# Optimization experiments

Measured on AMD Instinct MI355X. Metric: run time of the kernel, lower is better.

Reference implementation:

```python
import jax, jax.numpy as jnp
import numpy as np
import math

B, S, DM, H = 2, 2048, 1024, 16
DH = DM // H  # 64


def setup_inputs() -> dict:
    key = jax.random.key(0)
    ks = jax.random.split(key, 12)
    s = 1.0 / math.sqrt(DM)
    inp = {
        "key": jax.random.normal(ks[0], (B, S, DM), jnp.float32),
        "value": jax.random.normal(ks[1], (B, S, DM), jnp.float32),
        "query": jax.random.normal(ks[2], (B, S, DM), jnp.float32),
        # causal mask: True = masked out (matches masked_fill semantics)
        "mask": jnp.broadcast_to(~jnp.tril(jnp.ones((S, S), bool)), (B, S, S)),
        "Wk": jax.random.normal(ks[3], (DM, DM), jnp.float32) * s,
        "bk": jnp.zeros((DM,), jnp.float32),
        "Wv": jax.random.normal(ks[4], (DM, DM), jnp.float32) * s,
        "bv": jnp.zeros((DM,), jnp.float32),
        "Wq": jax.random.normal(ks[5], (DM, DM), jnp.float32) * s,
        "bq": jnp.zeros((DM,), jnp.float32),
        "Wo": jax.random.normal(ks[6], (DM, DM), jnp.float32) * s,
        "bo": jnp.zeros((DM,), jnp.float32),
    }
    return inp


def _split_heads(x):
    # [B, S, H*DH] -> [B, H, S, DH]
    b, s, _ = x.shape
    return x.reshape(b, s, H, DH).transpose(0, 2, 1, 3)


def reference(key, value, query, mask, Wk, bk, Wv, bv, Wq, bq, Wo, bo):
    key_up = _split_heads(key @ Wk.T + bk)      # [B,H,S,DH]
    value_up = _split_heads(value @ Wv.T + bv)  # [B,H,S,DH]
    query_up = _split_heads(query @ Wq.T + bq) / math.sqrt(DH)
    scores = jnp.einsum("bhqd,bhkd->bhqk", query_up, key_up)  # [B,H,S,S]
    scores = jnp.where(mask[:, None, :, :], jnp.float32(-1e18), scores)
    attn = jax.nn.softmax(scores, axis=-1)
    # dropout is identity in eval mode
    context = jnp.einsum("bhqk,bhkd->bhqd", attn, value_up)
    context = context.transpose(0, 2, 1, 3).reshape(key.shape[0], -1, H * DH)
    output = context @ Wo.T + bo                # [B,S,DM]
    top_attn = attn[:, 0, :, :]                 # [B,S,S]
    return output, top_attn
```

## Files before the change

### kernel.cpp

```cpp
#include <hip/hip_runtime.h>
#include <hip/hip_bf16.h>
#include <math.h>

#define B_ 2
#define S_ 2048
#define DM_ 1024
#define H_ 16
#define DH_ 64

using short8 = __attribute__((ext_vector_type(8))) short;
using f32x4  = __attribute__((ext_vector_type(4))) float;

typedef const __attribute__((address_space(1))) void* gas_cvp;
typedef __attribute__((address_space(3))) void* las_vp;

struct CvtJobs {
    const float* in[7];
    ushort* out[7];
};

__device__ __forceinline__ ushort f2bu(float x) {
    __hip_bfloat16 h = __float2bfloat16(x);
    return *(ushort*)&h;
}

__global__ __launch_bounds__(256) void cvt_bf16(CvtJobs jobs) {
    const int bid = blockIdx.x;
    int j, blk;
    if (bid < 6144) { j = bid >> 11; blk = bid & 2047; }
    else { const int r = bid - 6144; j = 3 + (r >> 9); blk = r & 511; }
    const int idx = (blk * 256 + threadIdx.x) * 8;
    const float* in = jobs.in[j];
    float4 a = *(const float4*)&in[idx];
    float4 b = *(const float4*)&in[idx + 4];
    ushort u[8];
    u[0] = f2bu(a.x); u[1] = f2bu(a.y); u[2] = f2bu(a.z); u[3] = f2bu(a.w);
    u[4] = f2bu(b.x); u[5] = f2bu(b.y); u[6] = f2bu(b.z); u[7] = f2bu(b.w);
    *(int4*)&jobs.out[j][idx] = *(int4*)u;
}

struct ProjJobs {
    const ushort* A[3];
    const ushort* W[3];
    const float* bias[3];
    ushort* C[3];
    float scale[3];
};

#define PSTAGE_A(buf, k0v)                                                     \
    {                                                                          \
        _Pragma("unroll")                                                      \
        for (int i = 0; i < 2; i++) {                                          \
            const int s   = i * 512 + tid;                                     \
            const int c   = s >> 8;                                            \
            const int row = s & 255;                                           \
            __builtin_amdgcn_global_load_lds(                                  \
                (gas_cvp)(Ag + (size_t)(i0 + row) * 1024 + (k0v) + c * 8),     \
                (las_vp)&SH[(buf) * 16384 + (i * 512 + w * 64) * 8], 16, 0, 0);\
        }                                                                      \
    }

#define PSTAGE_B(buf, k0v)                                                     \
    {                                                                          \
        _Pragma("unroll")                                                      \
        for (int i = 0; i < 2; i++) {                                          \
            const int s   = i * 512 + tid;                                     \
            const int c   = s >> 8;                                            \
            const int row = s & 255;                                           \
            __builtin_amdgcn_global_load_lds(                                  \
                (gas_cvp)(Wg + (size_t)(j0 + row) * 1024 + (k0v) + c * 8),     \
                (las_vp)&SH[(buf) * 16384 + 8192 + (i * 512 + w * 64) * 8],    \
                16, 0, 0);                                                     \
        }                                                                      \
    }

__global__ __launch_bounds__(512) void gemm_proj3(ProjJobs jobs)
{
    __shared__ ushort SH[65536];

    const int o   = blockIdx.x;
    const int swz = (o & 7) * 24 + (o >> 3);
    const int z   = swz >> 6;
    const int rem = swz & 63;
    const int by  = rem >> 2;
    const int bx  = rem & 3;

    const ushort* Ag = jobs.A[z];
    const ushort* Wg = jobs.W[z];
    const float* bias = jobs.bias[z];
    ushort* C = jobs.C[z];
    const float scale = jobs.scale[z];

    const int tid  = threadIdx.x;
    const int w    = tid >> 6;
    const int lane = tid & 63;
    const int g    = lane >> 4;
    const int lr   = lane & 15;
    const int wm   = w >> 2;
    const int wn   = w & 3;
    const int i0   = by * 256;
    const int j0   = bx * 256;

    f32x4 acc[8][4];
    #pragma unroll
    for (int m = 0; m < 8; m++)
        #pragma unroll
        for (int n = 0; n < 4; n++)
            #pragma unroll
            for (int jj = 0; jj < 4; jj++) acc[m][n][jj] = 0.f;

    PSTAGE_A(0, 0);  PSTAGE_B(0, 0);
    PSTAGE_A(1, 32); PSTAGE_B(1, 32);
    PSTAGE_A(2, 64); PSTAGE_B(2, 64);

    for (int kt = 0; kt < 32; kt++) {
        if (kt < 30)       asm volatile("s_waitcnt vmcnt(8)" ::: "memory");
        else if (kt == 30) asm volatile("s_waitcnt vmcnt(4)" ::: "memory");
        else               asm volatile("s_waitcnt vmcnt(0)" ::: "memory");
        __builtin_amdgcn_s_barrier();

        const int ab = (kt & 3) * 16384;

        short8 af[8], bf01[2];
        #pragma unroll
        for (int m = 0; m < 8; m++)
            af[m] = *(const short8*)&SH[ab + (g * 256 + wm * 128 + m * 16 + lr) * 8];
        #pragma unroll
        for (int n = 0; n < 2; n++)
            bf01[n] = *(const short8*)&SH[ab + 8192 + (g * 256 + wn * 64 + n * 16 + lr) * 8];
        if (kt + 3 < 32) PSTAGE_A((kt + 3) & 3, (kt + 3) * 32);

        __builtin_amdgcn_s_setprio(1);
        #pragma unroll
        for (int m = 0; m < 8; m++)
            #pragma unroll
            for (int n = 0; n < 2; n++)
                acc[m][n] = __builtin_amdgcn_mfma_f32_16x16x32_bf16(
                    af[m], bf01[n], acc[m][n], 0, 0, 0);
        __builtin_amdgcn_s_setprio(0);
        __builtin_amdgcn_s_barrier();

        short8 bf23[2];
        #pragma unroll
        for (int n = 0; n < 2; n++)
            bf23[n] = *(const short8*)&SH[ab + 8192 + (g * 256 + wn * 64 + (n + 2) * 16 + lr) * 8];
        if (kt + 3 < 32) PSTAGE_B((kt + 3) & 3, (kt + 3) * 32);

        __builtin_amdgcn_s_setprio(1);
        #pragma unroll
        for (int m = 0; m < 8; m++)
            #pragma unroll
            for (int n = 0; n < 2; n++)
                acc[m][n + 2] = __builtin_amdgcn_mfma_f32_16x16x32_bf16(
                    af[m], bf23[n], acc[m][n + 2], 0, 0, 0);
        __builtin_amdgcn_s_setprio(0);
    }

    const int colbase = j0 + wn * 64;
    const int rowbase = i0 + wm * 128;
    #pragma unroll
    for (int n = 0; n < 4; n++) {
        const int col = colbase + n * 16 + lr;
        const float bb = bias[col];
        const int hh = col >> 6;
        const int d = col & 63;
        #pragma unroll
        for (int m = 0; m < 8; m++) {
            const int rb = rowbase + m * 16 + g * 4;
            #pragma unroll
            for (int jj = 0; jj < 4; jj++) {
                const float v = (acc[m][n][jj] + bb) * scale;
                const int i = rb + jj;
                const int b = i >> 11;
                const int srow = i & 2047;
                C[(((size_t)b * H_ + hh) * S_ + srow) * DH_ + d] = f2bu(v);
            }
        }
    }
}

#define GEMM_STAGE_A(buf, k0v)                                                 \
    {                                                                          \
        _Pragma("unroll")                                                      \
        for (int i = 0; i < 2; i++) {                                          \
            const int s   = i * 256 + tid;                                     \
            const int c   = s >> 7;                                            \
            const int row = s & 127;                                           \
            __builtin_amdgcn_global_load_lds(                                  \
                (gas_cvp)(Ag + (size_t)(i0 + row) * 1024 + (k0v) + c * 8),     \
                (las_vp)&AsB[buf][0][(i * 256 + w * 64) * 8], 16, 0, 0);       \
        }                                                                      \
    }

#define GEMM_STAGE_B(buf, k0v)                                                 \
    {                                                                          \
        _Pragma("unroll")                                                      \
        for (int i = 0; i < 2; i++) {                                          \
            const int s   = i * 256 + tid;                                     \
            const int c   = s >> 7;                                            \
            const int row = s & 127;                                           \
            __builtin_amdgcn_global_load_lds(                                  \
                (gas_cvp)(Wg + (size_t)(j0 + row) * 1024 + (k0v) + c * 8),     \
                (las_vp)&AsB[buf][1][(i * 256 + w * 64) * 8], 16, 0, 0);       \
        }                                                                      \
    }

__global__ __launch_bounds__(512) void flash_mfma(
    const ushort* __restrict__ Qb, const ushort* __restrict__ Kb,
    const ushort* __restrict__ Vb, __hip_bfloat16* __restrict__ ctx,
    float* __restrict__ m0, float* __restrict__ l0)
{
    const int bid = blockIdx.x;
    const int xcd = bid & 7;
    const int t   = bid >> 3;
    const int P   = (t >> 3) * 8 + xcd;
    const int p   = t & 7;
    const int h   = P & 15;
    const int b   = P >> 4;

    const size_t hoff = ((size_t)b * H_ + h) * S_ * DH_;
    const ushort* Qh = Qb + hoff;
    const ushort* Kh = Kb + hoff;
    const ushort* Vh = Vb + hoff;

    __shared__ ushort Ks[64][72];
    __shared__ ushort Vt[64][72];
    __shared__ ushort Ps[8][16][72];

    const int tid  = threadIdx.x;
    const int w    = tid >> 6;
    const int lane = tid & 63;
    const int g    = lane >> 4;
    const int lr   = lane & 15;
    const int q0A  = p * 128 + w * 16;
    const int q0B  = (15 - p) * 128 + w * 16;
    const int diagA = (q0A + 15) >> 6;
    const int diagB = (q0B + 15) >> 6;
    const int nkt   = 2 * (16 - p);

    short8 qfA0, qfA1, qfB0, qfB1;
    {
        const ushort* qa = Qh + (size_t)(q0A + lr) * DH_ + g * 8;
        qfA0 = *(const short8*)(qa);
        qfA1 = *(const short8*)(qa + 32);
        const ushort* qb = Qh + (size_t)(q0B + lr) * DH_ + g * 8;
        qfB0 = *(const short8*)(qb);
        qfB1 = *(const short8*)(qb + 32);
    }

    f32x4 oA[4], oB[4];
    #pragma unroll
    for (int nc = 0; nc < 4; nc++) {
        oA[nc][0]=0.f; oA[nc][1]=0.f; oA[nc][2]=0.f; oA[nc][3]=0.f;
        oB[nc][0]=0.f; oB[nc][1]=0.f; oB[nc][2]=0.f; oB[nc][3]=0.f;
    }
    float mA = -1e30f, lA = 0.f;
    float mB = -1e30f, lB = 0.f;

    int4 pk = *(const int4*)(Kh + (size_t)lane * DH_ + w * 8);
    int4 pv = *(const int4*)(Vh + (size_t)lane * DH_ + w * 8);

    for (int kt = 0; kt < nkt; kt++) {
        const int kvb = kt * 64;
        __syncthreads();
        {
            *(int4*)&Ks[lane][w * 8] = pk;
            ushort vv[8];
            *(int4*)vv = pv;
            #pragma unroll
            for (int j2 = 0; j2 < 8; j2++) Vt[w * 8 + j2][lane] = vv[j2];
        }
        if (kt + 1 < nkt) {
            const size_t roff = (size_t)(kvb + 64 + lane) * DH_ + w * 8;
            pk = *(const int4*)(Kh + roff);
            pv = *(const int4*)(Vh + roff);
        }
        __syncthreads();

        #pragma unroll
        for (int u = 0; u < 2; u++) {
            const int diag = (u == 0) ? diagA : diagB;
            if (kt > diag) continue;
            const int q0w   = (u == 0) ? q0A : q0B;
            const short8 qf0 = (u == 0) ? qfA0 : qfB0;
            const short8 qf1 = (u == 0) ? qfA1 : qfB1;
            float& m_r = (u == 0) ? mA : mB;
            float& l_r = (u == 0) ? lA : lB;
            f32x4* o   = (u == 0) ? oA : oB;
            const int qglob = q0w + lr;

            f32x4 st[4];
            #pragma unroll
            for (int mt = 0; mt < 4; mt++) { st[mt][0]=0.f; st[mt][1]=0.f; st[mt][2]=0.f; st[mt][3]=0.f; }
            __builtin_amdgcn_s_setprio(1);
            #pragma unroll
            for (int mt = 0; mt < 4; mt++) {
                short8 ka = *(const short8*)&Ks[16 * mt + lr][8 * g];
                short8 kb = *(const short8*)&Ks[16 * mt + lr][32 + 8 * g];
                st[mt] = __builtin_amdgcn_mfma_f32_16x16x32_bf16(ka, qf0, st[mt], 0, 0, 0);
                st[mt] = __builtin_amdgcn_mfma_f32_16x16x32_bf16(kb, qf1, st[mt], 0, 0, 0);
            }
            __builtin_amdgcn_s_setprio(0);

            if (kt == diag) {
                #pragma unroll
                for (int mt = 0; mt < 4; mt++)
                    #pragma unroll
                    for (int jj = 0; jj < 4; jj++)
                        if (kvb + 16 * mt + 4 * g + jj > qglob) st[mt][jj] = -1e30f;
            }

            float pmax = st[0][0];
            #pragma unroll
            for (int mt = 0; mt < 4; mt++)
                #pragma unroll
                for (int jj = 0; jj < 4; jj++)
                    pmax = fmaxf(pmax, st[mt][jj]);
            pmax = fmaxf(pmax, __shfl_xor(pmax, 16));
            pmax = fmaxf(pmax, __shfl_xor(pmax, 32));

            const bool defer = __all(pmax - m_r <= 8.0f);
            float mnew = m_r, scv = 1.0f;
            if (!defer) {
                mnew = fmaxf(m_r, pmax);
                scv  = __expf(m_r - mnew);
            }

            float lsum = 0.f;
            #pragma unroll
            for (int mt = 0; mt < 4; mt++)
                #pragma unroll
                for (int jj = 0; jj < 4; jj++) {
                    st[mt][jj] = __expf(st[mt][jj] - mnew);
                    lsum += st[mt][jj];
                }
            lsum += __shfl_xor(lsum, 16);
            lsum += __shfl_xor(lsum, 32);
            l_r = l_r * scv + lsum;
            m_r = mnew;

            if (!defer) {
                float sc0 = __shfl(scv, 4 * g + 0);
                float sc1 = __shfl(scv, 4 * g + 1);
                float sc2 = __shfl(scv, 4 * g + 2);
                float sc3 = __shfl(scv, 4 * g + 3);
                #pragma unroll
                for (int nc = 0; nc < 4; nc++) {
                    o[nc][0] *= sc0; o[nc][1] *= sc1;
                    o[nc][2] *= sc2; o[nc][3] *= sc3;
                }
            }

            #pragma unroll
            for (int mt = 0; mt < 4; mt++) {
                ushort u4[4];
                #pragma unroll
                for (int jj = 0; jj < 4; jj++) u4[jj] = f2bu(st[mt][jj]);
                *(uint2*)&Ps[w][lr][16 * mt + 4 * g] = *(uint2*)u4;
            }

            short8 pa0 = *(const short8*)&Ps[w][lr][8 * g];
            short8 pa1 = *(const short8*)&Ps[w][lr][32 + 8 * g];
            __builtin_amdgcn_s_setprio(1);
            #pragma unroll
            for (int nc = 0; nc < 4; nc++) {
                short8 v0 = *(const short8*)&Vt[16 * nc + lr][8 * g];
                short8 v1 = *(const short8*)&Vt[16 * nc + lr][32 + 8 * g];
                o[nc] = __builtin_amdgcn_mfma_f32_16x16x32_bf16(pa0, v0, o[nc], 0, 0, 0);
                o[nc] = __builtin_amdgcn_mfma_f32_16x16x32_bf16(pa1, v1, o[nc], 0, 0, 0);
            }
            __builtin_amdgcn_s_setprio(0);
        }
    }

    #pragma unroll
    for (int u = 0; u < 2; u++) {
        const int q0w = (u == 0) ? q0A : q0B;
        const float m_r = (u == 0) ? mA : mB;
        const float l_r = (u == 0) ? lA : lB;
        const f32x4* o  = (u == 0) ? oA : oB;
        const float linv = 1.0f / l_r;
        float li0 = __shfl(linv, 4 * g + 0);
        float li1 = __shfl(linv, 4 * g + 1);
        float li2 = __shfl(linv, 4 * g + 2);
        float li3 = __shfl(linv, 4 * g + 3);
        #pragma unroll
        for (int reg = 0; reg < 4; reg++) {
            const int qrow = q0w + 4 * g + reg;
            const float li = (reg == 0) ? li0 : (reg == 1) ? li1 : (reg == 2) ? li2 : li3;
            __hip_bfloat16* cp = ctx + ((size_t)b * S_ + qrow) * DM_ + h * DH_;
            #pragma unroll
            for (int nc = 0; nc < 4; nc++)
                cp[16 * nc + lr] = __float2bfloat16(o[nc][reg] * li);
        }
        if (h == 0 && lane < 16) {
            m0[b * S_ + q0w + lane] = m_r;
            l0[b * S_ + q0w + lane] = l_r;
        }
    }
}

__global__ __launch_bounds__(256) void tail_fused(
    const ushort* __restrict__ ctxb, const ushort* __restrict__ Wg_,
    const float* __restrict__ bo, float* __restrict__ out,
    const ushort* __restrict__ Qb, const ushort* __restrict__ Kb,
    const float* __restrict__ m0, const float* __restrict__ l0,
    float* __restrict__ attn)
{
    __shared__ ushort AsB[3][2][4096];
    const int o = blockIdx.x;
    const int tid = threadIdx.x;
    const int w    = tid >> 6;
    const int lane = tid & 63;
    const int g    = lane >> 4;
    const int lr   = lane & 15;

    if (o < 256) {
        const int swz = (o & 7) * 32 + (o >> 3);
        const int by  = swz >> 3;
        const int bx  = swz & 7;
        const int wm  = w >> 1;
        const int wn  = w & 1;
        const int i0  = by * 128;
        const int j0  = bx * 128;
        const ushort* Ag = ctxb;
        const ushort* Wg = Wg_;

        f32x4 acc[4][4];
        #pragma unroll
        for (int m = 0; m < 4; m++)
            #pragma unroll
            for (int n = 0; n < 4; n++)
                #pragma unroll
                for (int jj = 0; jj < 4; jj++) acc[m][n][jj] = 0.f;

        int bufc = 0;
        GEMM_STAGE_A(0, 0);  GEMM_STAGE_B(0, 0);
        GEMM_STAGE_A(1, 32); GEMM_STAGE_B(1, 32);
        for (int k0 = 0; k0 < 1024; k0 += 32) {
            if (k0 + 32 < 1024)
                asm volatile("s_waitcnt vmcnt(4)" ::: "memory");
            else
                asm volatile("s_waitcnt vmcnt(0)" ::: "memory");
            __builtin_amdgcn_s_barrier();
            const int nb = (bufc + 2 >= 3) ? bufc - 1 : bufc + 2;

            short8 af[4], bf01[2];
            #pragma unroll
            for (int m = 0; m < 4; m++)
                af[m] = *(const short8*)&AsB[bufc][0][((g << 7) + wm * 64 + m * 16 + lr) * 8];
            #pragma unroll
            for (int n = 0; n < 2; n++)
                bf01[n] = *(const short8*)&AsB[bufc][1][((g << 7) + wn * 64 + n * 16 + lr) * 8];
            if (k0 + 64 < 1024) GEMM_STAGE_A(nb, k0 + 64);

            __builtin_amdgcn_s_setprio(1);
            #pragma unroll
            for (int m = 0; m < 4; m++)
                #pragma unroll
                for (int n = 0; n < 2; n++)
                    acc[m][n] = __builtin_amdgcn_mfma_f32_16x16x32_bf16(
                        af[m], bf01[n], acc[m][n], 0, 0, 0);
            __builtin_amdgcn_s_setprio(0);
            __builtin_amdgcn_s_barrier();

            short8 bf23[2];
            #pragma unroll
            for (int n = 0; n < 2; n++)
                bf23[n] = *(const short8*)&AsB[bufc][1][((g << 7) + wn * 64 + (n + 2) * 16 + lr) * 8];
            if (k0 + 64 < 1024) GEMM_STAGE_B(nb, k0 + 64);

            __builtin_amdgcn_s_setprio(1);
            #pragma unroll
            for (int m = 0; m < 4; m++)
                #pragma unroll
                for (int n = 0; n < 2; n++)
                    acc[m][n + 2] = __builtin_amdgcn_mfma_f32_16x16x32_bf16(
                        af[m], bf23[n], acc[m][n + 2], 0, 0, 0);
            __builtin_amdgcn_s_setprio(0);

            bufc = (bufc + 1 == 3) ? 0 : bufc + 1;
        }

        const int colbase = j0 + wn * 64;
        const int rowbase = i0 + wm * 64;
        #pragma unroll
        for (int n = 0; n < 4; n++) {
            const int col = colbase + n * 16 + lr;
            const float bb = bo[col];
            #pragma unroll
            for (int m = 0; m < 4; m++) {
                const int rb = rowbase + m * 16 + g * 4;
                #pragma unroll
                for (int jj = 0; jj < 4; jj++)
                    out[(size_t)(rb + jj) * DM_ + col] = acc[m][n][jj] + bb;
            }
        }
        return;
    }

    const int t   = o - 256;
    const int kt  = t & 31;
    const int qt2 = (t >> 5) & 31;
    const int b   = t >> 10;
    float* ap = attn + (size_t)b * S_ * S_;

    if (kt > qt2) {
        const int row = qt2 * 64 + (tid >> 2);
        const int col = kt * 64 + (tid & 3) * 16;
        float4 z = {0.f, 0.f, 0.f, 0.f};
        float* rp = ap + (size_t)row * S_ + col;
        *(float4*)&rp[0]  = z;
        *(float4*)&rp[4]  = z;
        *(float4*)&rp[8]  = z;
        *(float4*)&rp[12] = z;
        return;
    }

    ushort (*Ks)[72] = (ushort(*)[72])&AsB[0][0][0];
    const int q0w = qt2 * 64 + w * 16;
    const int kvb = kt * 64;
    const size_t hoff = (size_t)b * H_ * S_ * DH_;
    const ushort* Qh = Qb + hoff;
    const ushort* Kh = Kb + hoff;

    #pragma unroll
    for (int i = 0; i < 2; i++) {
        const int c = w + 4 * i;
        int4 k4 = *(const int4*)(Kh + (size_t)(kvb + lane) * DH_ + c * 8);
        *(int4*)&Ks[lane][c * 8] = k4;
    }

    short8 qf0, qf1;
    {
        const ushort* qp = Qh + (size_t)(q0w + lr) * DH_ + g * 8;
        qf0 = *(const short8*)(qp);
        qf1 = *(const short8*)(qp + 32);
    }
    const int qglob = q0w + lr;
    const float mv   = m0[b * S_ + qglob];
    const float linv = 1.0f / l0[b * S_ + qglob];
    __syncthreads();

    f32x4 st[4];
    #pragma unroll
    for (int mt = 0; mt < 4; mt++) { st[mt][0]=0.f; st[mt][1]=0.f; st[mt][2]=0.f; st[mt][3]=0.f; }
    #pragma unroll
    for (int mt = 0; mt < 4; mt++) {
        short8 ka = *(const short8*)&Ks[16 * mt + lr][8 * g];
        short8 kb = *(const short8*)&Ks[16 * mt + lr][32 + 8 * g];
        st[mt] = __builtin_amdgcn_mfma_f32_16x16x32_bf16(ka, qf0, st[mt], 0, 0, 0);
        st[mt] = __builtin_amdgcn_mfma_f32_16x16x32_bf16(kb, qf1, st[mt], 0, 0, 0);
    }

    float* rowp = ap + (size_t)qglob * S_ + kvb;
    #pragma unroll
    for (int mt = 0; mt < 4; mt++) {
        float4 ov;
        float v[4];
        #pragma unroll
        for (int jj = 0; jj < 4; jj++) {
            const int kv = 16 * mt + 4 * g + jj;
            float pv = __expf(st[mt][jj] - mv) * linv;
            v[jj] = (kvb + kv > qglob) ? 0.f : pv;
        }
        ov.x = v[0]; ov.y = v[1]; ov.z = v[2]; ov.w = v[3];
        *(float4*)&rowp[16 * mt + 4 * g] = ov;
    }
}

extern "C" void kernel_launch(void* const* d_in, const int* in_sizes, int n_in,
                              void* d_out, int out_size, void* d_ws, size_t ws_size,
                              hipStream_t stream)
{
    const float* key   = (const float*)d_in[0];
    const float* value = (const float*)d_in[1];
    const float* query = (const float*)d_in[2];
    const float* Wk = (const float*)d_in[4];
    const float* bk = (const float*)d_in[5];
    const float* Wv = (const float*)d_in[6];
    const float* bv = (const float*)d_in[7];
    const float* Wq = (const float*)d_in[8];
    const float* bq = (const float*)d_in[9];
    const float* Wo = (const float*)d_in[10];
    const float* bo = (const float*)d_in[11];

    char* ws = (char*)d_ws;
    const size_t per = (size_t)B_ * H_ * S_ * DH_;
    const size_t wsz = (size_t)DM_ * DM_;
    __hip_bfloat16* Qp   = (__hip_bfloat16*)ws;
    __hip_bfloat16* Kp   = Qp + per;
    __hip_bfloat16* Vp   = Kp + per;
    __hip_bfloat16* ctxb = Vp + per;
    __hip_bfloat16* qc   = ctxb + per;
    __hip_bfloat16* kc   = qc + per;
    __hip_bfloat16* vc   = kc + per;
    __hip_bfloat16* wqb  = vc + per;
    __hip_bfloat16* wkb  = wqb + wsz;
    __hip_bfloat16* wvb  = wkb + wsz;
    __hip_bfloat16* wob  = wvb + wsz;
    float* m0 = (float*)(wob + wsz);
    float* l0 = m0 + B_ * S_;

    float* out   = (float*)d_out;
    float* topat = out + (size_t)B_ * S_ * DM_;

    CvtJobs jobs;
    jobs.in[0] = query; jobs.out[0] = (ushort*)qc;
    jobs.in[1] = key;   jobs.out[1] = (ushort*)kc;
    jobs.in[2] = value; jobs.out[2] = (ushort*)vc;
    jobs.in[3] = Wq;    jobs.out[3] = (ushort*)wqb;
    jobs.in[4] = Wk;    jobs.out[4] = (ushort*)wkb;
    jobs.in[5] = Wv;    jobs.out[5] = (ushort*)wvb;
    jobs.in[6] = Wo;    jobs.out[6] = (ushort*)wob;
    cvt_bf16<<<6144 + 4 * 512, 256, 0, stream>>>(jobs);

    ProjJobs pj;
    pj.A[0] = (const ushort*)qc; pj.W[0] = (const ushort*)wqb; pj.bias[0] = bq;
    pj.C[0] = (ushort*)Qp; pj.scale[0] = 0.125f;
    pj.A[1] = (const ushort*)kc; pj.W[1] = (const ushort*)wkb; pj.bias[1] = bk;
    pj.C[1] = (ushort*)Kp; pj.scale[1] = 1.0f;
    pj.A[2] = (const ushort*)vc; pj.W[2] = (const ushort*)wvb; pj.bias[2] = bv;
    pj.C[2] = (ushort*)Vp; pj.scale[2] = 1.0f;
    gemm_proj3<<<192, 512, 0, stream>>>(pj);

    flash_mfma<<<256, 512, 0, stream>>>(
        (const ushort*)Qp, (const ushort*)Kp, (const ushort*)Vp, ctxb, m0, l0);

    tail_fused<<<256 + B_ * 32 * 32, 256, 0, stream>>>(
        (const ushort*)ctxb, (const ushort*)wob, bo, out,
        (const ushort*)Qp, (const ushort*)Kp, m0, l0, topat);
}
```

Baseline: 137.7 us.

## Split flash attention KV range in two halves and merge with combine kernel

The flash attention kernel now splits each block's key range into two halves processed by separate blocks, doubling the grid from 256 to 512. Each half writes unnormalized bf16 partial outputs plus row max and sum into reused workspace buffers. A new combine kernel merges the two partials with log-sum-exp rescaling and writes ctx and the head-0 stats. This aims to fill more compute units, at the cost of an extra launch, extra global traffic and bf16 rounding of the unnormalized partials.

```diff
diff --git a/kernel.cpp b/kernel.cpp
--- a/kernel.cpp
+++ b/kernel.cpp
@@ -207,16 +207,23 @@
 
 __global__ __launch_bounds__(512) void flash_mfma(
     const ushort* __restrict__ Qb, const ushort* __restrict__ Kb,
-    const ushort* __restrict__ Vb, __hip_bfloat16* __restrict__ ctx,
-    float* __restrict__ m0, float* __restrict__ l0)
+    const ushort* __restrict__ Vb,
+    ushort* __restrict__ po0, ushort* __restrict__ po1,
+    float* __restrict__ pm0, float* __restrict__ pm1,
+    float* __restrict__ pl0, float* __restrict__ pl1)
 {
     const int bid = blockIdx.x;
     const int xcd = bid & 7;
     const int t   = bid >> 3;
-    const int P   = (t >> 3) * 8 + xcd;
+    const int P   = (t >> 4) * 8 + xcd;
+    const int s   = (t >> 3) & 1;
     const int p   = t & 7;
     const int h   = P & 15;
     const int b   = P >> 4;
+
+    ushort* po = s ? po1 : po0;
+    float*  pm = s ? pm1 : pm0;
+    float*  pl = s ? pl1 : pl0;
 
     const size_t hoff = ((size_t)b * H_ + h) * S_ * DH_;
     const ushort* Qh = Qb + hoff;
@@ -236,7 +243,9 @@
     const int q0B  = (15 - p) * 128 + w * 16;
     const int diagA = (q0A + 15) >> 6;
     const int diagB = (q0B + 15) >> 6;
-    const int nkt   = 2 * (16 - p);
+    const int h0    = 16 - p;
+    const int ks    = s * h0;
+    const int ke    = ks + h0;
 
     short8 qfA0, qfA1, qfB0, qfB1;
     {
@@ -257,10 +266,10 @@
     float mA = -1e30f, lA = 0.f;
     float mB = -1e30f, lB = 0.f;
 
-    int4 pk = *(const int4*)(Kh + (size_t)lane * DH_ + w * 8);
-    int4 pv = *(const int4*)(Vh + (size_t)lane * DH_ + w * 8);
-
-    for (int kt = 0; kt < nkt; kt++) {
+    int4 pk = *(const int4*)(Kh + (size_t)(ks * 64 + lane) * DH_ + w * 8);
+    int4 pv = *(const int4*)(Vh + (size_t)(ks * 64 + lane) * DH_ + w * 8);
+
+    for (int kt = ks; kt < ke; kt++) {
         const int kvb = kt * 64;
         __syncthreads();
         {
@@ -270,7 +279,7 @@
             #pragma unroll
             for (int j2 = 0; j2 < 8; j2++) Vt[w * 8 + j2][lane] = vv[j2];
         }
-        if (kt + 1 < nkt) {
+        if (kt + 1 < ke) {
             const size_t roff = (size_t)(kvb + 64 + lane) * DH_ + w * 8;
             pk = *(const int4*)(Kh + roff);
             pv = *(const int4*)(Vh + roff);
@@ -379,24 +388,57 @@
         const float m_r = (u == 0) ? mA : mB;
         const float l_r = (u == 0) ? lA : lB;
         const f32x4* o  = (u == 0) ? oA : oB;
-        const float linv = 1.0f / l_r;
-        float li0 = __shfl(linv, 4 * g + 0);
-        float li1 = __shfl(linv, 4 * g + 1);
-        float li2 = __shfl(linv, 4 * g + 2);
-        float li3 = __shfl(linv, 4 * g + 3);
         #pragma unroll
         for (int reg = 0; reg < 4; reg++) {
             const int qrow = q0w + 4 * g + reg;
-            const float li = (reg == 0) ? li0 : (reg == 1) ? li1 : (reg == 2) ? li2 : li3;
-            __hip_bfloat16* cp = ctx + ((size_t)b * S_ + qrow) * DM_ + h * DH_;
+            ushort* cp = po + ((size_t)P * S_ + qrow) * 64;
             #pragma unroll
             for (int nc = 0; nc < 4; nc++)
-                cp[16 * nc + lr] = __float2bfloat16(o[nc][reg] * li);
-        }
-        if (h == 0 && lane < 16) {
-            m0[b * S_ + q0w + lane] = m_r;
-            l0[b * S_ + q0w + lane] = l_r;
-        }
+                cp[16 * nc + lr] = f2bu(o[nc][reg]);
+        }
+        if (lane < 16) {
+            pm[(size_t)P * S_ + q0w + lane] = m_r;
+            pl[(size_t)P * S_ + q0w + lane] = l_r;
+        }
+    }
+}
+
+__global__ __launch_bounds__(256) void flash_combine(
+    const ushort* __restrict__ po0, const ushort* __restrict__ po1,
+    const float* __restrict__ pm0, const float* __restrict__ pm1,
+    const float* __restrict__ pl0, const float* __restrict__ pl1,
+    ushort* __restrict__ ctx, float* __restrict__ m0, float* __restrict__ l0)
+{
+    const int t   = threadIdx.x;
+    const int row = blockIdx.x * 8 + (t >> 5);
+    const int d0  = (t & 31) * 2;
+    const int P = row >> 11;
+    const int q = row & 2047;
+    const int h = P & 15;
+    const int b = P >> 4;
+
+    const float m1 = pm0[row], m2 = pm1[row];
+    const float l1 = pl0[row], l2 = pl1[row];
+    const float m  = fmaxf(m1, m2);
+    const float f1 = __expf(m1 - m);
+    const float f2 = __expf(m2 - m);
+    const float l  = l1 * f1 + l2 * f2;
+    const float inv = 1.0f / l;
+
+    const uint a = *(const uint*)&po0[(size_t)row * 64 + d0];
+    const uint c = *(const uint*)&po1[(size_t)row * 64 + d0];
+    const float a0 = __uint_as_float((a & 0xffffu) << 16);
+    const float a1 = __uint_as_float((a >> 16) << 16);
+    const float c0 = __uint_as_float((c & 0xffffu) << 16);
+    const float c1 = __uint_as_float((c >> 16) << 16);
+    ushort r[2];
+    r[0] = f2bu((a0 * f1 + c0 * f2) * inv);
+    r[1] = f2bu((a1 * f1 + c1 * f2) * inv);
+    *(uint*)&ctx[((size_t)b * S_ + q) * DM_ + h * 64 + d0] = *(uint*)r;
+
+    if ((t & 31) == 0 && h == 0) {
+        m0[b * S_ + q] = m;
+        l0[b * S_ + q] = l;
     }
 }
 
@@ -601,6 +643,10 @@
     __hip_bfloat16* wob  = wvb + wsz;
     float* m0 = (float*)(wob + wsz);
     float* l0 = m0 + B_ * S_;
+    float* pm0 = l0 + B_ * S_;
+    float* pm1 = pm0 + 32 * S_;
+    float* pl0 = pm1 + 32 * S_;
+    float* pl1 = pl0 + 32 * S_;
 
     float* out   = (float*)d_out;
     float* topat = out + (size_t)B_ * S_ * DM_;
@@ -624,8 +670,13 @@
     pj.C[2] = (ushort*)Vp; pj.scale[2] = 1.0f;
     gemm_proj3<<<192, 512, 0, stream>>>(pj);
 
-    flash_mfma<<<256, 512, 0, stream>>>(
-        (const ushort*)Qp, (const ushort*)Kp, (const ushort*)Vp, ctxb, m0, l0);
+    flash_mfma<<<512, 512, 0, stream>>>(
+        (const ushort*)Qp, (const ushort*)Kp, (const ushort*)Vp,
+        (ushort*)qc, (ushort*)kc, pm0, pm1, pl0, pl1);
+
+    flash_combine<<<(32 * S_) / 8, 256, 0, stream>>>(
+        (const ushort*)qc, (const ushort*)kc, pm0, pm1, pl0, pl1,
+        (ushort*)ctxb, m0, l0);
 
     tail_fused<<<256 + B_ * 32 * 32, 256, 0, stream>>>(
         (const ushort*)ctxb, (const ushort*)wob, bo, out,
```

New measurement: 140.7 us. 2.2% more time.
